# Kernel tuning notes

Measured on AMD Instinct MI355X. Metric: run time of the kernel, lower is better.

The kernel has to match this reference:

```python
import jax, jax.numpy as jnp
import numpy as np
from jax import lax

T, B, S, A, H = 64, 256, 1024, 32, 2048


def setup_inputs() -> dict:
    key = jax.random.key(0)
    ks = jax.random.split(key, 9)
    sc = lambda n: 1.0 / np.sqrt(n)
    return {
        "prev_state": jax.random.normal(ks[0], (B, S), jnp.float32),
        "actions": jax.random.normal(ks[1], (T, B, A), jnp.float32),
        "prev_belief": jax.random.normal(ks[2], (B, H), jnp.float32),
        "eps": jax.random.normal(ks[3], (T, B, S), jnp.float32),
        "W_ih": jax.random.normal(ks[4], (3 * H, H), jnp.float32) * sc(H),
        "W_hh": jax.random.normal(ks[5], (3 * H, H), jnp.float32) * sc(H),
        "b_ih": jnp.zeros((3 * H,), jnp.float32),
        "b_hh": jnp.zeros((3 * H,), jnp.float32),
        "W_tp": jax.random.normal(ks[6], (S + A, H), jnp.float32) * sc(S + A),
        "b_tp": jnp.zeros((H,), jnp.float32),
        "W_post": jax.random.normal(ks[7], (H, 2 * S), jnp.float32) * sc(H),
        "b_post": jnp.zeros((2 * S,), jnp.float32),
    }


def reference(prev_state, actions, prev_belief, eps, W_ih, W_hh, b_ih, b_hh,
              W_tp, b_tp, W_post, b_post):
    def step(carry, inp):
        state, belief = carry
        a, e = inp
        # hidden = relu(transition_pre([state, action]))
        hidden = jax.nn.relu(jnp.concatenate([state, a], axis=-1) @ W_tp + b_tp)
        # torch GRUCell: h' = (1-z)*n + z*h
        gi = hidden @ W_ih.T + b_ih  # [B, 3H]
        gh = belief @ W_hh.T + b_hh  # [B, 3H]
        ir, iz, i_n = jnp.split(gi, 3, axis=-1)
        hr, hz, h_n = jnp.split(gh, 3, axis=-1)
        r = jax.nn.sigmoid(ir + hr)
        z = jax.nn.sigmoid(iz + hz)
        n = jnp.tanh(i_n + r * h_n)
        new_belief = (1.0 - z) * n + z * belief
        # prior statistics from transition_post(hidden)
        mean, std_raw = jnp.split(hidden @ W_post + b_post, 2, axis=-1)
        std = jax.nn.softplus(std_raw)
        # diag MVN rsample == mean + std * eps
        new_state = mean + std * e
        return (new_state, new_belief), (new_belief, new_state, mean, std)

    _, ys = lax.scan(step, (prev_state, prev_belief), (actions, eps))
    beliefs, prior_states, prior_means, prior_stds = ys  # each [T, B, ...]
    return beliefs, prior_states, prior_means, prior_stds
```

## Files before the change

kernel.cpp:

```cpp
#include <hip/hip_runtime.h>
#include <hip/hip_bf16.h>
#include <math.h>

constexpr int kT = 64, kB = 256, kS = 1024, kA = 32, kH = 2048;
constexpr int kH3 = 3 * kH;
constexpr int kS2 = 2 * kS;

typedef __hip_bfloat16 bf16;
typedef __bf16 bf16x8 __attribute__((ext_vector_type(8)));
typedef float f32x4 __attribute__((ext_vector_type(4)));

__device__ inline f32x4 mfma16(bf16x8 a, bf16x8 b, f32x4 c) {
  return __builtin_amdgcn_mfma_f32_16x16x32_bf16(a, b, c, 0, 0, 0);
}

__device__ inline void gload16(const void* g, void* l) {
  __builtin_amdgcn_global_load_lds(
      (const __attribute__((address_space(1))) void*)g,
      (__attribute__((address_space(3))) void*)l, 16, 0, 0);
}

#define PSYNC(vm)                                              \
  do {                                                         \
    asm volatile("s_waitcnt vmcnt(" #vm ")" ::: "memory");     \
    __builtin_amdgcn_sched_barrier(0);                         \
    __builtin_amdgcn_s_barrier();                              \
    __builtin_amdgcn_sched_barrier(0);                         \
  } while (0)


template<int ROWS>
__device__ __forceinline__ void stage32(const bf16* __restrict__ g, int ldK, bf16* lds) {
  const int tid = threadIdx.x;
#pragma unroll
  for (int i = 0; i < ROWS / 64; ++i) {
    const int idx = i * 256 + tid;
    const int r = idx >> 2;
    const int cc = (idx & 3) ^ ((r >> 1) & 3);
    gload16(g + (size_t)r * ldK + cc * 8, lds + (size_t)(i * 4 + (tid >> 6)) * 512);
  }
}

__device__ __forceinline__ void stage32_pair(const bf16* __restrict__ gM,
                                             const bf16* __restrict__ gS, int ldK,
                                             bf16* ldsM, bf16* ldsS) {
  const int tid = threadIdx.x;
  const int half = tid >> 7;
  const int t2 = tid & 127;
  const int r = t2 >> 2;
  const int cc = (t2 & 3) ^ ((r >> 1) & 3);
  const bf16* src = half ? gS : gM;
  bf16* dst = (half ? ldsS : ldsM) + ((tid >> 6) & 1) * 512;
  gload16(src + (size_t)r * ldK + cc * 8, dst);
}

__device__ __forceinline__ bf16x8 ldfrag32(const bf16* lds, int row0) {
  const int lane = threadIdx.x & 63;
  const int row = row0 + (lane & 15);
  const int c = (lane >> 4) ^ ((row >> 1) & 3);
  return *reinterpret_cast<const bf16x8*>(lds + row * 32 + c * 8);
}


__global__ void k_zero(unsigned* p, int n) {
  int i = blockIdx.x * 64 + threadIdx.x;
  if (i < n) p[i] = 0u;
}

__global__ void k_cvt(const float* __restrict__ src, bf16* __restrict__ dst, int n) {
  int i = (blockIdx.x * 256 + threadIdx.x) * 4;
  if (i >= n) return;
  float4 v = *reinterpret_cast<const float4*>(src + i);
  dst[i + 0] = __float2bfloat16(v.x);
  dst[i + 1] = __float2bfloat16(v.y);
  dst[i + 2] = __float2bfloat16(v.z);
  dst[i + 3] = __float2bfloat16(v.w);
}

__global__ void k_cvt_belief(const float* __restrict__ src, bf16* __restrict__ dstb,
                             float* __restrict__ dstf, int n) {
  int i = (blockIdx.x * 256 + threadIdx.x) * 4;
  if (i >= n) return;
  float4 v = *reinterpret_cast<const float4*>(src + i);
  dstb[i + 0] = __float2bfloat16(v.x);
  dstb[i + 1] = __float2bfloat16(v.y);
  dstb[i + 2] = __float2bfloat16(v.z);
  dstb[i + 3] = __float2bfloat16(v.w);
  *reinterpret_cast<float4*>(dstf + i) = v;
}

__global__ __launch_bounds__(256) void k_transpose(const float* __restrict__ src,
                                                   bf16* __restrict__ dst, int R, int C) {
  __shared__ float tile[32][33];
  const int c0 = blockIdx.x * 32, r0 = blockIdx.y * 32;
  const int tx = threadIdx.x & 31, ty = threadIdx.x >> 5;
#pragma unroll
  for (int i = 0; i < 32; i += 8)
    tile[ty + i][tx] = src[(size_t)(r0 + ty + i) * C + c0 + tx];
  __syncthreads();
#pragma unroll
  for (int i = 0; i < 32; i += 8)
    dst[(size_t)(c0 + ty + i) * R + r0 + tx] = __float2bfloat16(tile[tx][ty + i]);
}

__global__ __launch_bounds__(256) void k_actb(const float* __restrict__ actions,
                                              const float* __restrict__ Wtpa,
                                              const float* __restrict__ b_tp,
                                              bf16* __restrict__ actb) {
  __shared__ float a_s[64][32];
  const int tb0 = blockIdx.x * 64;
  const int tid = threadIdx.x;
  for (int i = tid; i < 64 * 32 / 4; i += 256) {
    float4 v = *reinterpret_cast<const float4*>(actions + (size_t)tb0 * 32 + i * 4);
    reinterpret_cast<float4*>(&a_s[0][0])[i] = v;
  }
  __syncthreads();
#pragma unroll
  for (int j = 0; j < 8; ++j) {
    const int c = j * 256 + tid;
    float w[32];
#pragma unroll
    for (int a = 0; a < 32; ++a) w[a] = Wtpa[a * kH + c];
    const float bt = b_tp[c];
    for (int r = 0; r < 64; ++r) {
      float acc = bt;
#pragma unroll
      for (int a = 0; a < 32; ++a) acc += a_s[r][a] * w[a];
      actb[(size_t)(tb0 + r) * kH + c] = __float2bfloat16(acc);
    }
  }
}


__global__ __launch_bounds__(256, 2) void k_mega(
    bf16* __restrict__ stateb, const bf16* __restrict__ WtpT,
    const bf16* __restrict__ actb_t, bf16* __restrict__ hidW,
    int doHidden, int waitPost,
    const bf16* __restrict__ hidR, const bf16* __restrict__ WpostT,
    const float* __restrict__ b_post, const float* __restrict__ eps_t,
    float* __restrict__ means_t, float* __restrict__ stds_t,
    float* __restrict__ states_t, int doPost,
    const bf16* __restrict__ Wih, const float* __restrict__ b_ih,
    bf16* __restrict__ GIw, int doGi,
    const bf16* __restrict__ Whh, const float* __restrict__ b_hh,
    const bf16* __restrict__ GIr, float* __restrict__ belief_f32,
    float* __restrict__ outB, const bf16* __restrict__ bbA,
    bf16* __restrict__ bbB, int doGru,
    unsigned* __restrict__ flags) {
  __shared__ __align__(16) bf16 smem[32768];
  const int bx = blockIdx.x;
  const int xcd = bx & 7, j = bx >> 3;
  const int tid = threadIdx.x, wv = tid >> 6, lane = tid & 63;
  const int l16 = lane & 15, k8 = lane >> 4;
  const int wr = (wv >> 1) * 32, wc = (wv & 1) * 32;

  if (j < 16) {
    if (!doHidden) return;
    const int n0 = xcd * 256 + (j & 3) * 64, m0 = (j >> 2) * 64;
    if (waitPost) {
      if (tid == 0) {
        unsigned* f = flags + (m0 >> 6) * 32;
        while (__hip_atomic_fetch_add(f, 0u, __ATOMIC_RELAXED,
                                      __HIP_MEMORY_SCOPE_AGENT) < 32u)
          __builtin_amdgcn_s_sleep(16);
      }
      __syncthreads();
    }
    const bf16* Ag = stateb + (size_t)m0 * kS;
    const bf16* Bg = WtpT + (size_t)n0 * kS;
    f32x4 acc[2][2] = {};
#define STG_H(t, s)                                            \
  {                                                            \
    stage32<64>(Ag + (t) * 32, kS, smem + (s) * 4096);         \
    stage32<64>(Bg + (t) * 32, kS, smem + (s) * 4096 + 2048);  \
  }
    STG_H(0, 0); STG_H(1, 1); STG_H(2, 2);
    for (int kt = 0; kt < 32; ++kt) {
      if (kt < 30) PSYNC(4);
      else if (kt == 30) PSYNC(2);
      else PSYNC(0);
      if (kt + 3 < 32) STG_H(kt + 3, (kt + 3) & 3);
      const bf16* As = smem + (kt & 3) * 4096;
      const bf16* Bs = As + 2048;
      bf16x8 a0 = ldfrag32(As, wr), a1 = ldfrag32(As, wr + 16);
      bf16x8 b0 = ldfrag32(Bs, wc), b1 = ldfrag32(Bs, wc + 16);
      acc[0][0] = mfma16(a0, b0, acc[0][0]);
      acc[0][1] = mfma16(a0, b1, acc[0][1]);
      acc[1][0] = mfma16(a1, b0, acc[1][0]);
      acc[1][1] = mfma16(a1, b1, acc[1][1]);
    }
#undef STG_H
#pragma unroll
    for (int mi = 0; mi < 2; ++mi)
#pragma unroll
      for (int ni = 0; ni < 2; ++ni)
#pragma unroll
        for (int ii = 0; ii < 4; ++ii) {
          int row = m0 + wr + mi * 16 + k8 * 4 + ii;
          int col = n0 + wc + ni * 16 + l16;
          float h = acc[mi][ni][ii] + __bfloat162float(actb_t[(size_t)row * kH + col]);
          hidW[(size_t)row * kH + col] = __float2bfloat16(fmaxf(h, 0.f));
        }
  } else if (j < 32) {
    if (!doGru) return;
    const int jj = j - 16;
    const int n0 = xcd * 256 + (jj & 3) * 64, m0 = (jj >> 2) * 64;
    const bf16* Ag = bbA + (size_t)m0 * kH;
    const bf16* G0 = Whh + (size_t)(0 * kH + n0) * kH;
    const bf16* G1 = Whh + (size_t)(1 * kH + n0) * kH;
    const bf16* G2 = Whh + (size_t)(2 * kH + n0) * kH;
    f32x4 acc[3][2][2] = {};
#define STG_G(t, s)                                            \
  {                                                            \
    stage32<64>(Ag + (t) * 32, kH, smem + (s) * 8192);         \
    stage32<64>(G0 + (t) * 32, kH, smem + (s) * 8192 + 2048);  \
    stage32<64>(G1 + (t) * 32, kH, smem + (s) * 8192 + 4096);  \
    stage32<64>(G2 + (t) * 32, kH, smem + (s) * 8192 + 6144);  \
  }
    STG_G(0, 0); STG_G(1, 1); STG_G(2, 2);
    for (int kt = 0; kt < 64; ++kt) {
      if (kt < 62) PSYNC(8);
      else if (kt == 62) PSYNC(4);
      else PSYNC(0);
      if (kt + 3 < 64) STG_G(kt + 3, (kt + 3) & 3);
      const bf16* As = smem + (kt & 3) * 8192;
      bf16x8 a0 = ldfrag32(As, wr), a1 = ldfrag32(As, wr + 16);
#pragma unroll
      for (int g = 0; g < 3; ++g) {
        const bf16* Bs = As + 2048 * (1 + g);
        bf16x8 b0 = ldfrag32(Bs, wc), b1 = ldfrag32(Bs, wc + 16);
        acc[g][0][0] = mfma16(a0, b0, acc[g][0][0]);
        acc[g][0][1] = mfma16(a0, b1, acc[g][0][1]);
        acc[g][1][0] = mfma16(a1, b0, acc[g][1][0]);
        acc[g][1][1] = mfma16(a1, b1, acc[g][1][1]);
      }
    }
#undef STG_G
#pragma unroll
    for (int mi = 0; mi < 2; ++mi)
#pragma unroll
      for (int ni = 0; ni < 2; ++ni)
#pragma unroll
        for (int ii = 0; ii < 4; ++ii) {
          int row = m0 + wr + mi * 16 + k8 * 4 + ii;
          int col = n0 + wc + ni * 16 + l16;
          const bf16* gi = GIr + (size_t)row * kH3;
          float hr = acc[0][mi][ni][ii] + b_hh[col];
          float hz = acc[1][mi][ni][ii] + b_hh[kH + col];
          float hn = acc[2][mi][ni][ii] + b_hh[2 * kH + col];
          float r = 1.f / (1.f + expf(-(__bfloat162float(gi[col]) + hr)));
          float z = 1.f / (1.f + expf(-(__bfloat162float(gi[kH + col]) + hz)));
          float n = tanhf(__bfloat162float(gi[2 * kH + col]) + r * hn);
          float bel = belief_f32[(size_t)row * kH + col];
          float nb = (1.f - z) * n + z * bel;
          outB[(size_t)row * kH + col] = nb;
          belief_f32[(size_t)row * kH + col] = nb;
          bbB[(size_t)row * kH + col] = __float2bfloat16(nb);
        }
  } else if (j < 48) {
    if (!doPost) return;
    const int jj = j - 32;
    const int p0 = xcd * 128 + (jj & 3) * 32, m0 = (jj >> 2) * 64;
    const int wpc = (wv & 1) * 16;
    const bf16* Ag = hidR + (size_t)m0 * kH;
    const bf16* Mg = WpostT + (size_t)p0 * kH;
    const bf16* Sg = WpostT + (size_t)(kS + p0) * kH;
    f32x4 accM[2] = {}, accS[2] = {};
#define STG_P(t, s)                                                        \
  {                                                                        \
    stage32<64>(Ag + (t) * 32, kH, smem + (s) * 4096);                     \
    stage32_pair(Mg + (t) * 32, Sg + (t) * 32, kH,                         \
                 smem + (s) * 4096 + 2048, smem + (s) * 4096 + 3072);      \
  }
    STG_P(0, 0); STG_P(1, 1); STG_P(2, 2);
    for (int kt = 0; kt < 64; ++kt) {
      if (kt < 62) PSYNC(4);
      else if (kt == 62) PSYNC(2);
      else PSYNC(0);
      if (kt + 3 < 64) STG_P(kt + 3, (kt + 3) & 3);
      const bf16* As = smem + (kt & 3) * 4096;
      bf16x8 a0 = ldfrag32(As, wr), a1 = ldfrag32(As, wr + 16);
      bf16x8 bm = ldfrag32(As + 2048, wpc);
      bf16x8 bs = ldfrag32(As + 3072, wpc);
      accM[0] = mfma16(a0, bm, accM[0]);
      accM[1] = mfma16(a1, bm, accM[1]);
      accS[0] = mfma16(a0, bs, accS[0]);
      accS[1] = mfma16(a1, bs, accS[1]);
    }
#undef STG_P
#pragma unroll
    for (int mi = 0; mi < 2; ++mi)
#pragma unroll
      for (int ii = 0; ii < 4; ++ii) {
        int row = m0 + wr + mi * 16 + k8 * 4 + ii;
        int p = p0 + wpc + l16;
        float mean = accM[mi][ii] + b_post[p];
        float sraw = accS[mi][ii] + b_post[kS + p];
        float sp = (sraw > 20.f) ? sraw : log1pf(expf(sraw));
        float sv = mean + sp * eps_t[(size_t)row * kS + p];
        means_t[(size_t)row * kS + p] = mean;
        stds_t[(size_t)row * kS + p] = sp;
        states_t[(size_t)row * kS + p] = sv;
        __hip_bfloat16 hb = __float2bfloat16(sv);
        unsigned ub = *reinterpret_cast<unsigned short*>(&hb);
        const bf16* ap = stateb + (size_t)row * kS + p;
        asm volatile("global_store_short %0, %1, off sc0 sc1"
                     :: "v"(ap), "v"(ub) : "memory");
      }
    asm volatile("s_waitcnt vmcnt(0)" ::: "memory");
    __syncthreads();
    if (tid == 0)
      __hip_atomic_fetch_add(flags + (m0 >> 6) * 32, 1u, __ATOMIC_RELAXED,
                             __HIP_MEMORY_SCOPE_AGENT);
  } else {
    if (!doGi) return;
    const int jj = j - 48;
    const int n0 = xcd * 768 + (jj % 6) * 128;
    const int m0 = (jj / 6) * 128;
    const int wrg = (wv >> 1) * 64, wcg = (wv & 1) * 64;
    const bf16* Ag = hidR + (size_t)m0 * kH;
    const bf16* Bg = Wih + (size_t)n0 * kH;
    f32x4 acc[4][4] = {};
#define STG_I(t, s)                                             \
  {                                                             \
    stage32<128>(Ag + (t) * 32, kH, smem + (s) * 8192);         \
    stage32<128>(Bg + (t) * 32, kH, smem + (s) * 8192 + 4096);  \
  }
    STG_I(0, 0); STG_I(1, 1); STG_I(2, 2);
    for (int kt = 0; kt < 64; ++kt) {
      if (kt < 62) PSYNC(8);
      else if (kt == 62) PSYNC(4);
      else PSYNC(0);
      if (kt + 3 < 64) STG_I(kt + 3, (kt + 3) & 3);
      const bf16* As = smem + (kt & 3) * 8192;
      const bf16* Bs = As + 4096;
      bf16x8 a[4], b[4];
#pragma unroll
      for (int i = 0; i < 4; ++i) a[i] = ldfrag32(As, wrg + i * 16);
#pragma unroll
      for (int i = 0; i < 4; ++i) b[i] = ldfrag32(Bs, wcg + i * 16);
#pragma unroll
      for (int mi = 0; mi < 4; ++mi)
#pragma unroll
        for (int ni = 0; ni < 4; ++ni)
          acc[mi][ni] = mfma16(a[mi], b[ni], acc[mi][ni]);
    }
#undef STG_I
#pragma unroll
    for (int mi = 0; mi < 4; ++mi)
#pragma unroll
      for (int ni = 0; ni < 4; ++ni)
#pragma unroll
        for (int ii = 0; ii < 4; ++ii) {
          int row = m0 + wrg + mi * 16 + k8 * 4 + ii;
          int col = n0 + wcg + ni * 16 + l16;
          GIw[(size_t)row * kH3 + col] = __float2bfloat16(acc[mi][ni][ii] + b_ih[col]);
        }
  }
}


extern "C" void kernel_launch(void* const* d_in, const int* in_sizes, int n_in,
                              void* d_out, int out_size, void* d_ws, size_t ws_size,
                              hipStream_t stream) {
  const float* prev_state  = (const float*)d_in[0];
  const float* actions     = (const float*)d_in[1];
  const float* prev_belief = (const float*)d_in[2];
  const float* eps         = (const float*)d_in[3];
  const float* W_ih        = (const float*)d_in[4];
  const float* W_hh        = (const float*)d_in[5];
  const float* b_ih        = (const float*)d_in[6];
  const float* b_hh        = (const float*)d_in[7];
  const float* W_tp        = (const float*)d_in[8];
  const float* b_tp        = (const float*)d_in[9];
  const float* W_post      = (const float*)d_in[10];
  const float* b_post      = (const float*)d_in[11];

  float* out_beliefs = (float*)d_out;
  float* out_states  = out_beliefs + (size_t)kT * kB * kH;
  float* out_means   = out_states + (size_t)kT * kB * kS;
  float* out_stds    = out_means + (size_t)kT * kB * kS;

  size_t off = 0;
  auto alloc = [&](size_t bytes) {
    void* r = (char*)d_ws + off;
    off += (bytes + 255) & ~(size_t)255;
    return r;
  };
  const int nFlagWords = (kT + 2) * 4 * 32;
  unsigned* flags = (unsigned*)alloc((size_t)nFlagWords * sizeof(unsigned));
  bf16* Wih_b  = (bf16*)alloc((size_t)kH3 * kH * 2);
  bf16* Whh_b  = (bf16*)alloc((size_t)kH3 * kH * 2);
  bf16* WtpT   = (bf16*)alloc((size_t)kH * kS * 2);
  bf16* WpostT = (bf16*)alloc((size_t)kS2 * kH * 2);
  bf16* actb   = (bf16*)alloc((size_t)kT * kB * kH * 2);
  bf16* hid0   = (bf16*)alloc((size_t)kB * kH * 2);
  bf16* hid1   = (bf16*)alloc((size_t)kB * kH * 2);
  bf16* hid[2] = {hid0, hid1};
  bf16* stateb = (bf16*)alloc((size_t)kB * kS * 2);
  bf16* bb0    = (bf16*)alloc((size_t)kB * kH * 2);
  bf16* bb1    = (bf16*)alloc((size_t)kB * kH * 2);
  bf16* bb[2]  = {bb0, bb1};
  float* belief_f32 = (float*)alloc((size_t)kB * kH * 4);
  bf16* GI = (bf16*)alloc((size_t)2 * kB * kH3 * 2);

  k_zero<<<dim3((nFlagWords + 63) / 64), dim3(64), 0, stream>>>(flags, nFlagWords);
  k_cvt<<<dim3(kH3 * kH / 1024), 256, 0, stream>>>(W_ih, Wih_b, kH3 * kH);
  k_cvt<<<dim3(kH3 * kH / 1024), 256, 0, stream>>>(W_hh, Whh_b, kH3 * kH);
  k_cvt<<<dim3(kB * kS / 1024), 256, 0, stream>>>(prev_state, stateb, kB * kS);
  k_cvt_belief<<<dim3(kB * kH / 1024), 256, 0, stream>>>(prev_belief, bb0, belief_f32, kB * kH);
  k_transpose<<<dim3(kH / 32, kS / 32), 256, 0, stream>>>(W_tp, WtpT, kS, kH);
  k_transpose<<<dim3(kS2 / 32, kH / 32), 256, 0, stream>>>(W_post, WpostT, kH, kS2);
  k_actb<<<dim3(kT * kB / 64), 256, 0, stream>>>(actions, W_tp + (size_t)kS * kH, b_tp, actb);

  auto mega = [&](int u, int doH, int doP, int doGi, int doGru) {
    const int up = (u > 0) ? u - 1 : 0;
    const int ug = (u > 1) ? u - 2 : 0;
    k_mega<<<dim3(480), dim3(256), 0, stream>>>(
        stateb, WtpT, actb + (size_t)(doH ? u : 0) * kB * kH, hid[u & 1],
        doH, doP,
        hid[(u + 1) & 1], WpostT, b_post, eps + (size_t)up * kB * kS,
        out_means + (size_t)up * kB * kS, out_stds + (size_t)up * kB * kS,
        out_states + (size_t)up * kB * kS, doP,
        Wih_b, b_ih, GI + (size_t)((u + 1) & 1) * kB * kH3, doGi,
        Whh_b, b_hh, GI + (size_t)(u & 1) * kB * kH3, belief_f32,
        out_beliefs + (size_t)ug * kB * kH, bb[u & 1], bb[(u + 1) & 1], doGru,
        flags + (size_t)4 * 32 * u);
  };
  for (int u = 0; u < kT; ++u) mega(u, 1, u > 0, u > 0, u >= 2);
  mega(kT, 0, 1, 1, 1);
  mega(kT + 1, 0, 0, 0, 1);
}
```

Baseline: 2.536 ms.

## Replace per-step kernel launches with persistent flag-synchronized multi-step kernel

Collapses the 66 per-timestep mega-kernel launches into a persistent kernel that loops over time steps. Each role (hidden, GRU, posterior, input-gate GEMMs) waits on and posts fine-grained per-row-block flags, so stages of different timesteps can overlap without launch boundaries. Intermediate buffers become ring buffers sized to workspace, and stores use write-through to make data visible across blocks. This removes launch and grid-drain overhead, at the cost of spin-waiting and relying on all 480 blocks being co-resident to avoid deadlock.

```diff
diff --git a/kernel.cpp b/kernel.cpp
--- a/kernel.cpp
+++ b/kernel.cpp
@@ -27,6 +27,29 @@
     __builtin_amdgcn_s_barrier();                              \
     __builtin_amdgcn_sched_barrier(0);                         \
   } while (0)
+
+__device__ __forceinline__ void store_wt(const bf16* p, float v) {
+  __hip_bfloat16 hb = __float2bfloat16(v);
+  unsigned ub = *reinterpret_cast<unsigned short*>(&hb);
+  asm volatile("global_store_short %0, %1, off sc0 sc1"
+               :: "v"(p), "v"(ub) : "memory");
+}
+
+__device__ __forceinline__ void poll_flag(unsigned* f, unsigned tgt) {
+  if (threadIdx.x == 0) {
+    while (__hip_atomic_fetch_add(f, 0u, __ATOMIC_RELAXED,
+                                  __HIP_MEMORY_SCOPE_AGENT) < tgt)
+      __builtin_amdgcn_s_sleep(8);
+  }
+  __syncthreads();
+}
+__device__ __forceinline__ void post_flag(unsigned* f) {
+  if (threadIdx.x == 0) {
+    __hip_atomic_fetch_add(f, 1u, __ATOMIC_RELAXED, __HIP_MEMORY_SCOPE_AGENT);
+    asm volatile("s_waitcnt vmcnt(0)" ::: "memory");
+  }
+}
+#define FLG(u, idx) (flags + ((size_t)(u) * 16 + (idx)) * 32)
 
 
 template<int ROWS>
@@ -63,7 +86,7 @@
 
 
 __global__ void k_zero(unsigned* p, int n) {
-  int i = blockIdx.x * 64 + threadIdx.x;
+  int i = blockIdx.x * 256 + threadIdx.x;
   if (i < n) p[i] = 0u;
 }
 
@@ -132,20 +155,18 @@
 }
 
 
-__global__ __launch_bounds__(256, 2) void k_mega(
-    bf16* __restrict__ stateb, const bf16* __restrict__ WtpT,
-    const bf16* __restrict__ actb_t, bf16* __restrict__ hidW,
-    int doHidden, int waitPost,
-    const bf16* __restrict__ hidR, const bf16* __restrict__ WpostT,
-    const float* __restrict__ b_post, const float* __restrict__ eps_t,
-    float* __restrict__ means_t, float* __restrict__ stds_t,
-    float* __restrict__ states_t, int doPost,
-    const bf16* __restrict__ Wih, const float* __restrict__ b_ih,
-    bf16* __restrict__ GIw, int doGi,
-    const bf16* __restrict__ Whh, const float* __restrict__ b_hh,
-    const bf16* __restrict__ GIr, float* __restrict__ belief_f32,
-    float* __restrict__ outB, const bf16* __restrict__ bbA,
-    bf16* __restrict__ bbB, int doGru,
+__global__ __launch_bounds__(256, 2) void k_seq(
+    int u0, int nsteps, int smask,
+    const bf16* __restrict__ WtpT, const bf16* __restrict__ Wih,
+    const bf16* __restrict__ Whh, const bf16* __restrict__ WpostT,
+    const float* __restrict__ b_ih, const float* __restrict__ b_hh,
+    const float* __restrict__ b_post,
+    const bf16* __restrict__ actb, const float* __restrict__ eps,
+    bf16* __restrict__ stR, bf16* __restrict__ hidR,
+    bf16* __restrict__ bbR, bf16* __restrict__ GIR,
+    float* __restrict__ belief_f32,
+    float* __restrict__ out_beliefs, float* __restrict__ out_states,
+    float* __restrict__ out_means, float* __restrict__ out_stds,
     unsigned* __restrict__ flags) {
   __shared__ __align__(16) bf16 smem[32768];
   const int bx = blockIdx.x;
@@ -153,63 +174,65 @@
   const int tid = threadIdx.x, wv = tid >> 6, lane = tid & 63;
   const int l16 = lane & 15, k8 = lane >> 4;
   const int wr = (wv >> 1) * 32, wc = (wv & 1) * 32;
+  const int uEnd = u0 + nsteps;
 
   if (j < 16) {
-    if (!doHidden) return;
-    const int n0 = xcd * 256 + (j & 3) * 64, m0 = (j >> 2) * 64;
-    if (waitPost) {
-      if (tid == 0) {
-        unsigned* f = flags + (m0 >> 6) * 32;
-        while (__hip_atomic_fetch_add(f, 0u, __ATOMIC_RELAXED,
-                                      __HIP_MEMORY_SCOPE_AGENT) < 32u)
-          __builtin_amdgcn_s_sleep(16);
-      }
-      __syncthreads();
-    }
-    const bf16* Ag = stateb + (size_t)m0 * kS;
+    const int m = j >> 2, m0 = m * 64;
+    const int n0 = xcd * 256 + (j & 3) * 64;
     const bf16* Bg = WtpT + (size_t)n0 * kS;
-    f32x4 acc[2][2] = {};
+    for (int u = u0; u < uEnd; ++u) {
+      if (u > 0) poll_flag(FLG(u, 4 + m), 32);
+      const bf16* Ag = stR + (size_t)(u & smask) * kB * kS + (size_t)m0 * kS;
+      f32x4 acc[2][2] = {};
 #define STG_H(t, s)                                            \
   {                                                            \
     stage32<64>(Ag + (t) * 32, kS, smem + (s) * 4096);         \
     stage32<64>(Bg + (t) * 32, kS, smem + (s) * 4096 + 2048);  \
   }
-    STG_H(0, 0); STG_H(1, 1); STG_H(2, 2);
-    for (int kt = 0; kt < 32; ++kt) {
-      if (kt < 30) PSYNC(4);
-      else if (kt == 30) PSYNC(2);
-      else PSYNC(0);
-      if (kt + 3 < 32) STG_H(kt + 3, (kt + 3) & 3);
-      const bf16* As = smem + (kt & 3) * 4096;
-      const bf16* Bs = As + 2048;
-      bf16x8 a0 = ldfrag32(As, wr), a1 = ldfrag32(As, wr + 16);
-      bf16x8 b0 = ldfrag32(Bs, wc), b1 = ldfrag32(Bs, wc + 16);
-      acc[0][0] = mfma16(a0, b0, acc[0][0]);
-      acc[0][1] = mfma16(a0, b1, acc[0][1]);
-      acc[1][0] = mfma16(a1, b0, acc[1][0]);
-      acc[1][1] = mfma16(a1, b1, acc[1][1]);
+      STG_H(0, 0); STG_H(1, 1); STG_H(2, 2);
+      for (int kt = 0; kt < 32; ++kt) {
+        if (kt < 30) PSYNC(4);
+        else if (kt == 30) PSYNC(2);
+        else PSYNC(0);
+        if (kt + 3 < 32) STG_H(kt + 3, (kt + 3) & 3);
+        const bf16* As = smem + (kt & 3) * 4096;
+        const bf16* Bs = As + 2048;
+        bf16x8 a0 = ldfrag32(As, wr), a1 = ldfrag32(As, wr + 16);
+        bf16x8 b0 = ldfrag32(Bs, wc), b1 = ldfrag32(Bs, wc + 16);
+        acc[0][0] = mfma16(a0, b0, acc[0][0]);
+        acc[0][1] = mfma16(a0, b1, acc[0][1]);
+        acc[1][0] = mfma16(a1, b0, acc[1][0]);
+        acc[1][1] = mfma16(a1, b1, acc[1][1]);
+      }
+#undef STG_H
+      const bf16* at = actb + (size_t)u * kB * kH;
+      bf16* hw = hidR + (size_t)(u & smask) * kB * kH;
+#pragma unroll
+      for (int mi = 0; mi < 2; ++mi)
+#pragma unroll
+        for (int ni = 0; ni < 2; ++ni)
+#pragma unroll
+          for (int ii = 0; ii < 4; ++ii) {
+            int row = m0 + wr + mi * 16 + k8 * 4 + ii;
+            int col = n0 + wc + ni * 16 + l16;
+            float h = acc[mi][ni][ii] + __bfloat162float(at[(size_t)row * kH + col]);
+            store_wt(hw + (size_t)row * kH + col, fmaxf(h, 0.f));
+          }
+      asm volatile("s_waitcnt vmcnt(0)" ::: "memory");
+      __syncthreads();
+      post_flag(FLG(u, 0 + m));
     }
-#undef STG_H
-#pragma unroll
-    for (int mi = 0; mi < 2; ++mi)
-#pragma unroll
-      for (int ni = 0; ni < 2; ++ni)
-#pragma unroll
-        for (int ii = 0; ii < 4; ++ii) {
-          int row = m0 + wr + mi * 16 + k8 * 4 + ii;
-          int col = n0 + wc + ni * 16 + l16;
-          float h = acc[mi][ni][ii] + __bfloat162float(actb_t[(size_t)row * kH + col]);
-          hidW[(size_t)row * kH + col] = __float2bfloat16(fmaxf(h, 0.f));
-        }
   } else if (j < 32) {
-    if (!doGru) return;
     const int jj = j - 16;
-    const int n0 = xcd * 256 + (jj & 3) * 64, m0 = (jj >> 2) * 64;
-    const bf16* Ag = bbA + (size_t)m0 * kH;
+    const int m = jj >> 2, mb = m >> 1, m0 = m * 64;
+    const int n0 = xcd * 256 + (jj & 3) * 64;
     const bf16* G0 = Whh + (size_t)(0 * kH + n0) * kH;
     const bf16* G1 = Whh + (size_t)(1 * kH + n0) * kH;
     const bf16* G2 = Whh + (size_t)(2 * kH + n0) * kH;
-    f32x4 acc[3][2][2] = {};
+    for (int u = u0; u < uEnd; ++u) {
+      if (u > 0) poll_flag(FLG(u - 1, 12 + m), 32);
+      const bf16* Ag = bbR + (size_t)(u & smask) * kB * kH + (size_t)m0 * kH;
+      f32x4 acc[3][2][2] = {};
 #define STG_G(t, s)                                            \
   {                                                            \
     stage32<64>(Ag + (t) * 32, kH, smem + (s) * 8192);         \
@@ -217,145 +240,162 @@
     stage32<64>(G1 + (t) * 32, kH, smem + (s) * 8192 + 4096);  \
     stage32<64>(G2 + (t) * 32, kH, smem + (s) * 8192 + 6144);  \
   }
-    STG_G(0, 0); STG_G(1, 1); STG_G(2, 2);
-    for (int kt = 0; kt < 64; ++kt) {
-      if (kt < 62) PSYNC(8);
-      else if (kt == 62) PSYNC(4);
-      else PSYNC(0);
-      if (kt + 3 < 64) STG_G(kt + 3, (kt + 3) & 3);
-      const bf16* As = smem + (kt & 3) * 8192;
-      bf16x8 a0 = ldfrag32(As, wr), a1 = ldfrag32(As, wr + 16);
-#pragma unroll
-      for (int g = 0; g < 3; ++g) {
-        const bf16* Bs = As + 2048 * (1 + g);
-        bf16x8 b0 = ldfrag32(Bs, wc), b1 = ldfrag32(Bs, wc + 16);
-        acc[g][0][0] = mfma16(a0, b0, acc[g][0][0]);
-        acc[g][0][1] = mfma16(a0, b1, acc[g][0][1]);
-        acc[g][1][0] = mfma16(a1, b0, acc[g][1][0]);
-        acc[g][1][1] = mfma16(a1, b1, acc[g][1][1]);
+      STG_G(0, 0); STG_G(1, 1); STG_G(2, 2);
+      for (int kt = 0; kt < 64; ++kt) {
+        if (kt < 62) PSYNC(8);
+        else if (kt == 62) PSYNC(4);
+        else PSYNC(0);
+        if (kt + 3 < 64) STG_G(kt + 3, (kt + 3) & 3);
+        const bf16* As = smem + (kt & 3) * 8192;
+        bf16x8 a0 = ldfrag32(As, wr), a1 = ldfrag32(As, wr + 16);
+#pragma unroll
+        for (int g = 0; g < 3; ++g) {
+          const bf16* Bs = As + 2048 * (1 + g);
+          bf16x8 b0 = ldfrag32(Bs, wc), b1 = ldfrag32(Bs, wc + 16);
+          acc[g][0][0] = mfma16(a0, b0, acc[g][0][0]);
+          acc[g][0][1] = mfma16(a0, b1, acc[g][0][1]);
+          acc[g][1][0] = mfma16(a1, b0, acc[g][1][0]);
+          acc[g][1][1] = mfma16(a1, b1, acc[g][1][1]);
+        }
       }
+#undef STG_G
+      poll_flag(FLG(u, 8 + mb), 48);
+      const bf16* gi = GIR + (size_t)(u & smask) * kB * kH3;
+      float* outB = out_beliefs + (size_t)u * kB * kH;
+      bf16* bw = bbR + (size_t)((u + 1) & smask) * kB * kH;
+#pragma unroll
+      for (int mi = 0; mi < 2; ++mi)
+#pragma unroll
+        for (int ni = 0; ni < 2; ++ni)
+#pragma unroll
+          for (int ii = 0; ii < 4; ++ii) {
+            int row = m0 + wr + mi * 16 + k8 * 4 + ii;
+            int col = n0 + wc + ni * 16 + l16;
+            const bf16* gr = gi + (size_t)row * kH3;
+            float hr = acc[0][mi][ni][ii] + b_hh[col];
+            float hz = acc[1][mi][ni][ii] + b_hh[kH + col];
+            float hn = acc[2][mi][ni][ii] + b_hh[2 * kH + col];
+            float r = 1.f / (1.f + expf(-(__bfloat162float(gr[col]) + hr)));
+            float z = 1.f / (1.f + expf(-(__bfloat162float(gr[kH + col]) + hz)));
+            float n = tanhf(__bfloat162float(gr[2 * kH + col]) + r * hn);
+            float bel = belief_f32[(size_t)row * kH + col];
+            float nb = (1.f - z) * n + z * bel;
+            outB[(size_t)row * kH + col] = nb;
+            belief_f32[(size_t)row * kH + col] = nb;
+            store_wt(bw + (size_t)row * kH + col, nb);
+          }
+      asm volatile("s_waitcnt vmcnt(0)" ::: "memory");
+      __syncthreads();
+      post_flag(FLG(u, 12 + m));
     }
-#undef STG_G
-#pragma unroll
-    for (int mi = 0; mi < 2; ++mi)
-#pragma unroll
-      for (int ni = 0; ni < 2; ++ni)
-#pragma unroll
-        for (int ii = 0; ii < 4; ++ii) {
-          int row = m0 + wr + mi * 16 + k8 * 4 + ii;
-          int col = n0 + wc + ni * 16 + l16;
-          const bf16* gi = GIr + (size_t)row * kH3;
-          float hr = acc[0][mi][ni][ii] + b_hh[col];
-          float hz = acc[1][mi][ni][ii] + b_hh[kH + col];
-          float hn = acc[2][mi][ni][ii] + b_hh[2 * kH + col];
-          float r = 1.f / (1.f + expf(-(__bfloat162float(gi[col]) + hr)));
-          float z = 1.f / (1.f + expf(-(__bfloat162float(gi[kH + col]) + hz)));
-          float n = tanhf(__bfloat162float(gi[2 * kH + col]) + r * hn);
-          float bel = belief_f32[(size_t)row * kH + col];
-          float nb = (1.f - z) * n + z * bel;
-          outB[(size_t)row * kH + col] = nb;
-          belief_f32[(size_t)row * kH + col] = nb;
-          bbB[(size_t)row * kH + col] = __float2bfloat16(nb);
-        }
   } else if (j < 48) {
-    if (!doPost) return;
     const int jj = j - 32;
-    const int p0 = xcd * 128 + (jj & 3) * 32, m0 = (jj >> 2) * 64;
+    const int m = jj >> 2, m0 = m * 64;
+    const int p0 = xcd * 128 + (jj & 3) * 32;
     const int wpc = (wv & 1) * 16;
-    const bf16* Ag = hidR + (size_t)m0 * kH;
     const bf16* Mg = WpostT + (size_t)p0 * kH;
     const bf16* Sg = WpostT + (size_t)(kS + p0) * kH;
-    f32x4 accM[2] = {}, accS[2] = {};
+    for (int u = u0; u < uEnd; ++u) {
+      poll_flag(FLG(u, 0 + m), 32);
+      const bf16* Ag = hidR + (size_t)(u & smask) * kB * kH + (size_t)m0 * kH;
+      f32x4 accM[2] = {}, accS[2] = {};
 #define STG_P(t, s)                                                        \
   {                                                                        \
     stage32<64>(Ag + (t) * 32, kH, smem + (s) * 4096);                     \
     stage32_pair(Mg + (t) * 32, Sg + (t) * 32, kH,                         \
                  smem + (s) * 4096 + 2048, smem + (s) * 4096 + 3072);      \
   }
-    STG_P(0, 0); STG_P(1, 1); STG_P(2, 2);
-    for (int kt = 0; kt < 64; ++kt) {
-      if (kt < 62) PSYNC(4);
-      else if (kt == 62) PSYNC(2);
-      else PSYNC(0);
-      if (kt + 3 < 64) STG_P(kt + 3, (kt + 3) & 3);
-      const bf16* As = smem + (kt & 3) * 4096;
-      bf16x8 a0 = ldfrag32(As, wr), a1 = ldfrag32(As, wr + 16);
-      bf16x8 bm = ldfrag32(As + 2048, wpc);
-      bf16x8 bs = ldfrag32(As + 3072, wpc);
-      accM[0] = mfma16(a0, bm, accM[0]);
-      accM[1] = mfma16(a1, bm, accM[1]);
-      accS[0] = mfma16(a0, bs, accS[0]);
-      accS[1] = mfma16(a1, bs, accS[1]);
+      STG_P(0, 0); STG_P(1, 1); STG_P(2, 2);
+      for (int kt = 0; kt < 64; ++kt) {
+        if (kt < 62) PSYNC(4);
+        else if (kt == 62) PSYNC(2);
+        else PSYNC(0);
+        if (kt + 3 < 64) STG_P(kt + 3, (kt + 3) & 3);
+        const bf16* As = smem + (kt & 3) * 4096;
+        bf16x8 a0 = ldfrag32(As, wr), a1 = ldfrag32(As, wr + 16);
+        bf16x8 bm = ldfrag32(As + 2048, wpc);
+        bf16x8 bs = ldfrag32(As + 3072, wpc);
+        accM[0] = mfma16(a0, bm, accM[0]);
+        accM[1] = mfma16(a1, bm, accM[1]);
+        accS[0] = mfma16(a0, bs, accS[0]);
+        accS[1] = mfma16(a1, bs, accS[1]);
+      }
+#undef STG_P
+      const float* et = eps + (size_t)u * kB * kS;
+      float* mt = out_means + (size_t)u * kB * kS;
+      float* sdt = out_stds + (size_t)u * kB * kS;
+      float* xt = out_states + (size_t)u * kB * kS;
+      bf16* sw = stR + (size_t)((u + 1) & smask) * kB * kS;
+#pragma unroll
+      for (int mi = 0; mi < 2; ++mi)
+#pragma unroll
+        for (int ii = 0; ii < 4; ++ii) {
+          int row = m0 + wr + mi * 16 + k8 * 4 + ii;
+          int p = p0 + wpc + l16;
+          float mean = accM[mi][ii] + b_post[p];
+          float sraw = accS[mi][ii] + b_post[kS + p];
+          float sp = (sraw > 20.f) ? sraw : log1pf(expf(sraw));
+          float sv = mean + sp * et[(size_t)row * kS + p];
+          mt[(size_t)row * kS + p] = mean;
+          sdt[(size_t)row * kS + p] = sp;
+          xt[(size_t)row * kS + p] = sv;
+          store_wt(sw + (size_t)row * kS + p, sv);
+        }
+      asm volatile("s_waitcnt vmcnt(0)" ::: "memory");
+      __syncthreads();
+      post_flag(FLG(u + 1, 4 + m));
     }
-#undef STG_P
-#pragma unroll
-    for (int mi = 0; mi < 2; ++mi)
-#pragma unroll
-      for (int ii = 0; ii < 4; ++ii) {
-        int row = m0 + wr + mi * 16 + k8 * 4 + ii;
-        int p = p0 + wpc + l16;
-        float mean = accM[mi][ii] + b_post[p];
-        float sraw = accS[mi][ii] + b_post[kS + p];
-        float sp = (sraw > 20.f) ? sraw : log1pf(expf(sraw));
-        float sv = mean + sp * eps_t[(size_t)row * kS + p];
-        means_t[(size_t)row * kS + p] = mean;
-        stds_t[(size_t)row * kS + p] = sp;
-        states_t[(size_t)row * kS + p] = sv;
-        __hip_bfloat16 hb = __float2bfloat16(sv);
-        unsigned ub = *reinterpret_cast<unsigned short*>(&hb);
-        const bf16* ap = stateb + (size_t)row * kS + p;
-        asm volatile("global_store_short %0, %1, off sc0 sc1"
-                     :: "v"(ap), "v"(ub) : "memory");
-      }
-    asm volatile("s_waitcnt vmcnt(0)" ::: "memory");
-    __syncthreads();
-    if (tid == 0)
-      __hip_atomic_fetch_add(flags + (m0 >> 6) * 32, 1u, __ATOMIC_RELAXED,
-                             __HIP_MEMORY_SCOPE_AGENT);
   } else {
-    if (!doGi) return;
     const int jj = j - 48;
+    const int mb = jj / 6, m0 = mb * 128;
     const int n0 = xcd * 768 + (jj % 6) * 128;
-    const int m0 = (jj / 6) * 128;
     const int wrg = (wv >> 1) * 64, wcg = (wv & 1) * 64;
-    const bf16* Ag = hidR + (size_t)m0 * kH;
     const bf16* Bg = Wih + (size_t)n0 * kH;
-    f32x4 acc[4][4] = {};
+    for (int u = u0; u < uEnd; ++u) {
+      poll_flag(FLG(u, 0 + 2 * mb), 32);
+      poll_flag(FLG(u, 1 + 2 * mb), 32);
+      const bf16* Ag = hidR + (size_t)(u & smask) * kB * kH + (size_t)m0 * kH;
+      f32x4 acc[4][4] = {};
 #define STG_I(t, s)                                             \
   {                                                             \
     stage32<128>(Ag + (t) * 32, kH, smem + (s) * 8192);         \
     stage32<128>(Bg + (t) * 32, kH, smem + (s) * 8192 + 4096);  \
   }
-    STG_I(0, 0); STG_I(1, 1); STG_I(2, 2);
-    for (int kt = 0; kt < 64; ++kt) {
-      if (kt < 62) PSYNC(8);
-      else if (kt == 62) PSYNC(4);
-      else PSYNC(0);
-      if (kt + 3 < 64) STG_I(kt + 3, (kt + 3) & 3);
-      const bf16* As = smem + (kt & 3) * 8192;
-      const bf16* Bs = As + 4096;
-      bf16x8 a[4], b[4];
-#pragma unroll
-      for (int i = 0; i < 4; ++i) a[i] = ldfrag32(As, wrg + i * 16);
-#pragma unroll
-      for (int i = 0; i < 4; ++i) b[i] = ldfrag32(Bs, wcg + i * 16);
+      STG_I(0, 0); STG_I(1, 1); STG_I(2, 2);
+      for (int kt = 0; kt < 64; ++kt) {
+        if (kt < 62) PSYNC(8);
+        else if (kt == 62) PSYNC(4);
+        else PSYNC(0);
+        if (kt + 3 < 64) STG_I(kt + 3, (kt + 3) & 3);
+        const bf16* As = smem + (kt & 3) * 8192;
+        const bf16* Bs = As + 4096;
+        bf16x8 a[4], b[4];
+#pragma unroll
+        for (int i = 0; i < 4; ++i) a[i] = ldfrag32(As, wrg + i * 16);
+#pragma unroll
+        for (int i = 0; i < 4; ++i) b[i] = ldfrag32(Bs, wcg + i * 16);
+#pragma unroll
+        for (int mi = 0; mi < 4; ++mi)
+#pragma unroll
+          for (int ni = 0; ni < 4; ++ni)
+            acc[mi][ni] = mfma16(a[mi], b[ni], acc[mi][ni]);
+      }
+#undef STG_I
+      bf16* gw = GIR + (size_t)(u & smask) * kB * kH3;
 #pragma unroll
       for (int mi = 0; mi < 4; ++mi)
 #pragma unroll
         for (int ni = 0; ni < 4; ++ni)
-          acc[mi][ni] = mfma16(a[mi], b[ni], acc[mi][ni]);
+#pragma unroll
+          for (int ii = 0; ii < 4; ++ii) {
+            int row = m0 + wrg + mi * 16 + k8 * 4 + ii;
+            int col = n0 + wcg + ni * 16 + l16;
+            store_wt(gw + (size_t)row * kH3 + col, acc[mi][ni][ii] + b_ih[col]);
+          }
+      asm volatile("s_waitcnt vmcnt(0)" ::: "memory");
+      __syncthreads();
+      post_flag(FLG(u, 8 + mb));
     }
-#undef STG_I
-#pragma unroll
-    for (int mi = 0; mi < 4; ++mi)
-#pragma unroll
-      for (int ni = 0; ni < 4; ++ni)
-#pragma unroll
-        for (int ii = 0; ii < 4; ++ii) {
-          int row = m0 + wrg + mi * 16 + k8 * 4 + ii;
-          int col = n0 + wcg + ni * 16 + l16;
-          GIw[(size_t)row * kH3 + col] = __float2bfloat16(acc[mi][ni][ii] + b_ih[col]);
-        }
   }
 }
 
@@ -387,47 +427,42 @@
     off += (bytes + 255) & ~(size_t)255;
     return r;
   };
-  const int nFlagWords = (kT + 2) * 4 * 32;
+  const int nFlagWords = (kT + 1) * 16 * 32;
   unsigned* flags = (unsigned*)alloc((size_t)nFlagWords * sizeof(unsigned));
   bf16* Wih_b  = (bf16*)alloc((size_t)kH3 * kH * 2);
   bf16* Whh_b  = (bf16*)alloc((size_t)kH3 * kH * 2);
   bf16* WtpT   = (bf16*)alloc((size_t)kH * kS * 2);
   bf16* WpostT = (bf16*)alloc((size_t)kS2 * kH * 2);
   bf16* actb   = (bf16*)alloc((size_t)kT * kB * kH * 2);
-  bf16* hid0   = (bf16*)alloc((size_t)kB * kH * 2);
-  bf16* hid1   = (bf16*)alloc((size_t)kB * kH * 2);
-  bf16* hid[2] = {hid0, hid1};
-  bf16* stateb = (bf16*)alloc((size_t)kB * kS * 2);
-  bf16* bb0    = (bf16*)alloc((size_t)kB * kH * 2);
-  bf16* bb1    = (bf16*)alloc((size_t)kB * kH * 2);
-  bf16* bb[2]  = {bb0, bb1};
   float* belief_f32 = (float*)alloc((size_t)kB * kH * 4);
-  bf16* GI = (bf16*)alloc((size_t)2 * kB * kH3 * 2);
-
-  k_zero<<<dim3((nFlagWords + 63) / 64), dim3(64), 0, stream>>>(flags, nFlagWords);
+
+  const size_t perStep = (size_t)kB * kS * 2
+                       + (size_t)kB * kH * 2
+                       + (size_t)kB * kH * 2
+                       + (size_t)kB * kH3 * 2;
+  int SEG = 64;
+  while (SEG > 1 && off + (size_t)SEG * perStep + (size_t)SEG * 1024 > ws_size)
+    SEG >>= 1;
+  const int smask = SEG - 1;
+  bf16* stR  = (bf16*)alloc((size_t)SEG * kB * kS * 2);
+  bf16* hidR = (bf16*)alloc((size_t)SEG * kB * kH * 2);
+  bf16* bbR  = (bf16*)alloc((size_t)SEG * kB * kH * 2);
+  bf16* GIR  = (bf16*)alloc((size_t)SEG * kB * kH3 * 2);
+
+  k_zero<<<dim3((nFlagWords + 255) / 256), 256, 0, stream>>>(flags, nFlagWords);
   k_cvt<<<dim3(kH3 * kH / 1024), 256, 0, stream>>>(W_ih, Wih_b, kH3 * kH);
   k_cvt<<<dim3(kH3 * kH / 1024), 256, 0, stream>>>(W_hh, Whh_b, kH3 * kH);
-  k_cvt<<<dim3(kB * kS / 1024), 256, 0, stream>>>(prev_state, stateb, kB * kS);
-  k_cvt_belief<<<dim3(kB * kH / 1024), 256, 0, stream>>>(prev_belief, bb0, belief_f32, kB * kH);
+  k_cvt<<<dim3(kB * kS / 1024), 256, 0, stream>>>(prev_state, stR, kB * kS);
+  k_cvt_belief<<<dim3(kB * kH / 1024), 256, 0, stream>>>(prev_belief, bbR, belief_f32, kB * kH);
   k_transpose<<<dim3(kH / 32, kS / 32), 256, 0, stream>>>(W_tp, WtpT, kS, kH);
   k_transpose<<<dim3(kS2 / 32, kH / 32), 256, 0, stream>>>(W_post, WpostT, kH, kS2);
   k_actb<<<dim3(kT * kB / 64), 256, 0, stream>>>(actions, W_tp + (size_t)kS * kH, b_tp, actb);
 
-  auto mega = [&](int u, int doH, int doP, int doGi, int doGru) {
-    const int up = (u > 0) ? u - 1 : 0;
-    const int ug = (u > 1) ? u - 2 : 0;
-    k_mega<<<dim3(480), dim3(256), 0, stream>>>(
-        stateb, WtpT, actb + (size_t)(doH ? u : 0) * kB * kH, hid[u & 1],
-        doH, doP,
-        hid[(u + 1) & 1], WpostT, b_post, eps + (size_t)up * kB * kS,
-        out_means + (size_t)up * kB * kS, out_stds + (size_t)up * kB * kS,
-        out_states + (size_t)up * kB * kS, doP,
-        Wih_b, b_ih, GI + (size_t)((u + 1) & 1) * kB * kH3, doGi,
-        Whh_b, b_hh, GI + (size_t)(u & 1) * kB * kH3, belief_f32,
-        out_beliefs + (size_t)ug * kB * kH, bb[u & 1], bb[(u + 1) & 1], doGru,
-        flags + (size_t)4 * 32 * u);
-  };
-  for (int u = 0; u < kT; ++u) mega(u, 1, u > 0, u > 0, u >= 2);
-  mega(kT, 0, 1, 1, 1);
-  mega(kT + 1, 0, 0, 0, 1);
-}
+  for (int s = 0; s < kT; s += SEG) {
+    k_seq<<<dim3(480), dim3(256), 0, stream>>>(
+        s, SEG, smask,
+        WtpT, Wih_b, Whh_b, WpostT, b_ih, b_hh, b_post, actb, eps,
+        stR, hidR, bbR, GIR, belief_f32,
+        out_beliefs, out_states, out_means, out_stds, flags);
+  }
+}
```

Result: slower. 3.030 ms (+19.5%).

## Batch two timesteps of input-gate GEMM per launch to reuse W_ih tiles

Applied to the files above, without the earlier changes.

The input-gate GEMM (hidden @ W_ih^T) now runs every other step and handles two timesteps per block, looping over two hidden buffers against the same W_ih column tile. The schedule is deepened by one stage, with four hidden and GI buffers and a GRU lag of three steps instead of two. The aim is to improve L2/cache reuse of W_ih, since the second pass re-reads the same weight tile, and to halve the number of launches that carry GI work. In exchange, GI blocks take twice as long on alternate steps, which may unbalance those launches, and one extra launch is added.

```diff
diff --git a/kernel.cpp b/kernel.cpp
--- a/kernel.cpp
+++ b/kernel.cpp
@@ -136,12 +136,13 @@
     bf16* __restrict__ stateb, const bf16* __restrict__ WtpT,
     const bf16* __restrict__ actb_t, bf16* __restrict__ hidW,
     int doHidden, int waitPost,
-    const bf16* __restrict__ hidR, const bf16* __restrict__ WpostT,
+    const bf16* __restrict__ hidP, const bf16* __restrict__ WpostT,
     const float* __restrict__ b_post, const float* __restrict__ eps_t,
     float* __restrict__ means_t, float* __restrict__ stds_t,
     float* __restrict__ states_t, int doPost,
     const bf16* __restrict__ Wih, const float* __restrict__ b_ih,
-    bf16* __restrict__ GIw, int doGi,
+    const bf16* __restrict__ hidA, bf16* __restrict__ GIwA,
+    const bf16* __restrict__ hidB, bf16* __restrict__ GIwB, int doGi,
     const bf16* __restrict__ Whh, const float* __restrict__ b_hh,
     const bf16* __restrict__ GIr, float* __restrict__ belief_f32,
     float* __restrict__ outB, const bf16* __restrict__ bbA,
@@ -262,7 +263,7 @@
     const int jj = j - 32;
     const int p0 = xcd * 128 + (jj & 3) * 32, m0 = (jj >> 2) * 64;
     const int wpc = (wv & 1) * 16;
-    const bf16* Ag = hidR + (size_t)m0 * kH;
+    const bf16* Ag = hidP + (size_t)m0 * kH;
     const bf16* Mg = WpostT + (size_t)p0 * kH;
     const bf16* Sg = WpostT + (size_t)(kS + p0) * kH;
     f32x4 accM[2] = {}, accS[2] = {};
@@ -318,44 +319,48 @@
     const int n0 = xcd * 768 + (jj % 6) * 128;
     const int m0 = (jj / 6) * 128;
     const int wrg = (wv >> 1) * 64, wcg = (wv & 1) * 64;
-    const bf16* Ag = hidR + (size_t)m0 * kH;
     const bf16* Bg = Wih + (size_t)n0 * kH;
-    f32x4 acc[4][4] = {};
+    for (int ss = 0; ss < 2; ++ss) {
+      const bf16* Ag = (ss ? hidB : hidA) + (size_t)m0 * kH;
+      bf16* GIw = ss ? GIwB : GIwA;
+      f32x4 acc[4][4] = {};
 #define STG_I(t, s)                                             \
   {                                                             \
     stage32<128>(Ag + (t) * 32, kH, smem + (s) * 8192);         \
     stage32<128>(Bg + (t) * 32, kH, smem + (s) * 8192 + 4096);  \
   }
-    STG_I(0, 0); STG_I(1, 1); STG_I(2, 2);
-    for (int kt = 0; kt < 64; ++kt) {
-      if (kt < 62) PSYNC(8);
-      else if (kt == 62) PSYNC(4);
-      else PSYNC(0);
-      if (kt + 3 < 64) STG_I(kt + 3, (kt + 3) & 3);
-      const bf16* As = smem + (kt & 3) * 8192;
-      const bf16* Bs = As + 4096;
-      bf16x8 a[4], b[4];
-#pragma unroll
-      for (int i = 0; i < 4; ++i) a[i] = ldfrag32(As, wrg + i * 16);
-#pragma unroll
-      for (int i = 0; i < 4; ++i) b[i] = ldfrag32(Bs, wcg + i * 16);
+      STG_I(0, 0); STG_I(1, 1); STG_I(2, 2);
+      for (int kt = 0; kt < 64; ++kt) {
+        if (kt < 62) PSYNC(8);
+        else if (kt == 62) PSYNC(4);
+        else PSYNC(0);
+        if (kt + 3 < 64) STG_I(kt + 3, (kt + 3) & 3);
+        const bf16* As = smem + (kt & 3) * 8192;
+        const bf16* Bs = As + 4096;
+        bf16x8 a[4], b[4];
+#pragma unroll
+        for (int i = 0; i < 4; ++i) a[i] = ldfrag32(As, wrg + i * 16);
+#pragma unroll
+        for (int i = 0; i < 4; ++i) b[i] = ldfrag32(Bs, wcg + i * 16);
+#pragma unroll
+        for (int mi = 0; mi < 4; ++mi)
+#pragma unroll
+          for (int ni = 0; ni < 4; ++ni)
+            acc[mi][ni] = mfma16(a[mi], b[ni], acc[mi][ni]);
+      }
+#undef STG_I
 #pragma unroll
       for (int mi = 0; mi < 4; ++mi)
 #pragma unroll
         for (int ni = 0; ni < 4; ++ni)
-          acc[mi][ni] = mfma16(a[mi], b[ni], acc[mi][ni]);
-    }
-#undef STG_I
-#pragma unroll
-    for (int mi = 0; mi < 4; ++mi)
-#pragma unroll
-      for (int ni = 0; ni < 4; ++ni)
-#pragma unroll
-        for (int ii = 0; ii < 4; ++ii) {
-          int row = m0 + wrg + mi * 16 + k8 * 4 + ii;
-          int col = n0 + wcg + ni * 16 + l16;
-          GIw[(size_t)row * kH3 + col] = __float2bfloat16(acc[mi][ni][ii] + b_ih[col]);
-        }
+#pragma unroll
+          for (int ii = 0; ii < 4; ++ii) {
+            int row = m0 + wrg + mi * 16 + k8 * 4 + ii;
+            int col = n0 + wcg + ni * 16 + l16;
+            GIw[(size_t)row * kH3 + col] = __float2bfloat16(acc[mi][ni][ii] + b_ih[col]);
+          }
+      __syncthreads();
+    }
   }
 }
 
@@ -387,22 +392,22 @@
     off += (bytes + 255) & ~(size_t)255;
     return r;
   };
-  const int nFlagWords = (kT + 2) * 4 * 32;
+  const int nFlagWords = (kT + 3) * 4 * 32;
   unsigned* flags = (unsigned*)alloc((size_t)nFlagWords * sizeof(unsigned));
   bf16* Wih_b  = (bf16*)alloc((size_t)kH3 * kH * 2);
   bf16* Whh_b  = (bf16*)alloc((size_t)kH3 * kH * 2);
   bf16* WtpT   = (bf16*)alloc((size_t)kH * kS * 2);
   bf16* WpostT = (bf16*)alloc((size_t)kS2 * kH * 2);
   bf16* actb   = (bf16*)alloc((size_t)kT * kB * kH * 2);
-  bf16* hid0   = (bf16*)alloc((size_t)kB * kH * 2);
-  bf16* hid1   = (bf16*)alloc((size_t)kB * kH * 2);
-  bf16* hid[2] = {hid0, hid1};
+  bf16* hid[4];
+  for (int i = 0; i < 4; ++i) hid[i] = (bf16*)alloc((size_t)kB * kH * 2);
   bf16* stateb = (bf16*)alloc((size_t)kB * kS * 2);
   bf16* bb0    = (bf16*)alloc((size_t)kB * kH * 2);
   bf16* bb1    = (bf16*)alloc((size_t)kB * kH * 2);
   bf16* bb[2]  = {bb0, bb1};
   float* belief_f32 = (float*)alloc((size_t)kB * kH * 4);
-  bf16* GI = (bf16*)alloc((size_t)2 * kB * kH3 * 2);
+  bf16* GI[4];
+  for (int i = 0; i < 4; ++i) GI[i] = (bf16*)alloc((size_t)kB * kH3 * 2);
 
   k_zero<<<dim3((nFlagWords + 63) / 64), dim3(64), 0, stream>>>(flags, nFlagWords);
   k_cvt<<<dim3(kH3 * kH / 1024), 256, 0, stream>>>(W_ih, Wih_b, kH3 * kH);
@@ -413,21 +418,26 @@
   k_transpose<<<dim3(kS2 / 32, kH / 32), 256, 0, stream>>>(W_post, WpostT, kH, kS2);
   k_actb<<<dim3(kT * kB / 64), 256, 0, stream>>>(actions, W_tp + (size_t)kS * kH, b_tp, actb);
 
-  auto mega = [&](int u, int doH, int doP, int doGi, int doGru) {
-    const int up = (u > 0) ? u - 1 : 0;
-    const int ug = (u > 1) ? u - 2 : 0;
+  auto mega = [&](int u) {
+    const int doH   = (u < kT);
+    const int doP   = (u >= 1 && u <= kT);
+    const int doGi  = ((u & 1) == 0 && u >= 2 && u <= kT);
+    const int doGru = (u >= 3 && u <= kT + 2);
+    const int up = doP ? u - 1 : 0;
+    const int uA = doGi ? u - 2 : 0;
+    const int uB = doGi ? u - 1 : 0;
+    const int v  = doGru ? u - 3 : 0;
     k_mega<<<dim3(480), dim3(256), 0, stream>>>(
-        stateb, WtpT, actb + (size_t)(doH ? u : 0) * kB * kH, hid[u & 1],
+        stateb, WtpT, actb + (size_t)(doH ? u : 0) * kB * kH, hid[u & 3],
         doH, doP,
-        hid[(u + 1) & 1], WpostT, b_post, eps + (size_t)up * kB * kS,
+        hid[up & 3], WpostT, b_post, eps + (size_t)up * kB * kS,
         out_means + (size_t)up * kB * kS, out_stds + (size_t)up * kB * kS,
         out_states + (size_t)up * kB * kS, doP,
-        Wih_b, b_ih, GI + (size_t)((u + 1) & 1) * kB * kH3, doGi,
-        Whh_b, b_hh, GI + (size_t)(u & 1) * kB * kH3, belief_f32,
-        out_beliefs + (size_t)ug * kB * kH, bb[u & 1], bb[(u + 1) & 1], doGru,
+        Wih_b, b_ih,
+        hid[uA & 3], GI[uA & 3], hid[uB & 3], GI[uB & 3], doGi,
+        Whh_b, b_hh, GI[v & 3], belief_f32,
+        out_beliefs + (size_t)v * kB * kH, bb[v & 1], bb[(v + 1) & 1], doGru,
         flags + (size_t)4 * 32 * u);
   };
-  for (int u = 0; u < kT; ++u) mega(u, 1, u > 0, u > 0, u >= 2);
-  mega(kT, 0, 1, 1, 1);
-  mega(kT + 1, 0, 0, 0, 1);
-}
+  for (int u = 0; u <= kT + 2; ++u) mega(u);
+}
```

New measurement: 3.050 ms. 1.2x slower.
